# Optimization experiments

Hardware: AMD Instinct MI355X
Metric: run time of the kernel (lower is better)

Reference implementation:

```python
import jax, jax.numpy as jnp
import numpy as np

MAX_POS = 1024  # max_pos_embed_distance
H = 12          # num_heads
D = 768         # input_dim == hidden_dim
P = D // H      # head_dim


def setup_inputs() -> dict:
    key = jax.random.key(0)
    ks = jax.random.split(key, 8)
    s = 1.0 / np.sqrt(D)
    return {
        "x": jax.random.normal(ks[0], (8, 1024, D), dtype=jnp.float32),
        "wq": jax.random.uniform(ks[1], (D, D), jnp.float32, -s, s),
        "bq": jax.random.uniform(ks[2], (D,), jnp.float32, -s, s),
        "wk": jax.random.uniform(ks[3], (D, D), jnp.float32, -s, s),
        "bk": jax.random.uniform(ks[4], (D,), jnp.float32, -s, s),
        "wv": jax.random.uniform(ks[5], (D, D), jnp.float32, -s, s),
        "bv": jax.random.uniform(ks[6], (D,), jnp.float32, -s, s),
        "dist_emb": jax.random.normal(ks[7], (2 * MAX_POS - 1, P), dtype=jnp.float32),
    }


def reference(x, wq, bq, wk, bk, wv, bv, dist_emb):
    b, n, _ = x.shape
    factor = 1.0 / np.sqrt(P)
    # q,k,v: [b, n, h, p]
    q = (x @ wq.T + bq).reshape(b, n, H, P)
    k = (x @ wk.T + bk).reshape(b, n, H, P)
    v = (x @ wv.T + bv).reshape(b, n, H, P)
    raw = jnp.einsum('bihd,bjhd->bhij', q, k)
    # relative-key bias: pos_emb[i, r] = dist_emb[i - r + MAX_POS - 1]
    dist = jnp.arange(n)[:, None] - jnp.arange(n)[None, :]
    pos_emb = dist_emb[dist + MAX_POS - 1]           # [n, n, p]
    raw = raw + jnp.einsum('bihd,ird->bhir', q, pos_emb)
    # NOTE: original scales AFTER adding relative scores
    attn = jax.nn.softmax(raw * factor, axis=-1)
    out = jnp.einsum('bhij,bjhp->bihp', attn, v)
    return out.reshape(b, n, -1)
```

## Files before the change

### kernel.cpp

```cpp
#include <hip/hip_runtime.h>
#include <hip/hip_bf16.h>

#define NH 12
#define HD 64
#define DM 768
#define SEQ 1024
#define BATCH 8

typedef __attribute__((ext_vector_type(8))) short bf16x8;
typedef __attribute__((ext_vector_type(4))) short s16x4;
typedef __attribute__((ext_vector_type(4))) float f32x4;

__device__ __forceinline__ short f2b(float x) {
    unsigned u = __float_as_uint(x);
    u += 0x7fffu + ((u >> 16) & 1u);
    return (short)(u >> 16);
}

#define MFMA(A, B, C) __builtin_amdgcn_mfma_f32_16x16x32_bf16(A, B, C, 0, 0, 0)

__global__ __launch_bounds__(256) void cvt_f32_bf16(
    const float* __restrict__ in, short* __restrict__ out, int n4)
{
    int i = blockIdx.x * 256 + threadIdx.x;
    if (i < n4) {
        f32x4 v = *(const f32x4*)(in + 4 * (size_t)i);
        s16x4 r;
        r[0] = f2b(v[0]); r[1] = f2b(v[1]); r[2] = f2b(v[2]); r[3] = f2b(v[3]);
        *(s16x4*)(out + 4 * (size_t)i) = r;
    }
}

__global__ __launch_bounds__(256, 4) void qkv_mfma(
    const short* __restrict__ xb,
    const short* __restrict__ wqb, const float* __restrict__ bq,
    const short* __restrict__ wkb, const float* __restrict__ bk,
    const short* __restrict__ wvb, const float* __restrict__ bv,
    short* __restrict__ qb, short* __restrict__ kb, short* __restrict__ vt)
{
    __shared__ short Xl[64][72];
    __shared__ short Wl[64][72];

    const int orig = blockIdx.x;
    const int sw   = (orig & 7) * 576 + (orig >> 3);
    const int t    = sw % 36;
    const int by   = t % 12;
    const int z    = t / 12;
    const int bx   = sw / 36;

    const short* wmat = (z == 0) ? wqb : (z == 1) ? wkb : wvb;
    const float* bias = (z == 0) ? bq : (z == 1) ? bk : bv;

    const int i0   = bx * 64;
    const int col0 = by * 64;
    const int tid  = threadIdx.x;
    const int lane = tid & 63;
    const int w    = tid >> 6;
    const int lg   = lane >> 4;
    const int lc   = lane & 15;

    f32x4 acc[4] = {};
    for (int k0 = 0; k0 < DM; k0 += 64) {
        __syncthreads();
        #pragma unroll
        for (int e = tid; e < 512; e += 256) {
            const int r = e >> 3, c8 = e & 7;
            *(bf16x8*)&Xl[r][c8 * 8] =
                *(const bf16x8*)&xb[(size_t)(i0 + r) * DM + k0 + c8 * 8];
            *(bf16x8*)&Wl[r][c8 * 8] =
                *(const bf16x8*)&wmat[(size_t)(col0 + r) * DM + k0 + c8 * 8];
        }
        __syncthreads();
        #pragma unroll
        for (int kh = 0; kh < 2; ++kh) {
            const bf16x8 a = *(const bf16x8*)&Xl[w * 16 + lc][kh * 32 + lg * 8];
            #pragma unroll
            for (int n = 0; n < 4; ++n) {
                const bf16x8 bfr = *(const bf16x8*)&Wl[n * 16 + lc][kh * 32 + lg * 8];
                acc[n] = MFMA(a, bfr, acc[n]);
            }
        }
    }

    if (z < 2) {
        short* outp = (z == 0) ? qb : kb;
        #pragma unroll
        for (int n = 0; n < 4; ++n) {
            const int c = col0 + n * 16 + lc;
            const float bi = bias[c];
            #pragma unroll
            for (int rr = 0; rr < 4; ++rr) {
                const int r = i0 + w * 16 + lg * 4 + rr;
                outp[(size_t)r * DM + c] = f2b(acc[n][rr] + bi);
            }
        }
    } else {
        #pragma unroll
        for (int n = 0; n < 4; ++n) {
            const int c = col0 + n * 16 + lc;
            const int h = c >> 6, d = c & 63;
            const float bi = bias[c];
            #pragma unroll
            for (int rr = 0; rr < 4; ++rr) {
                const int r  = i0 + w * 16 + lg * 4 + rr;
                const int bb = r >> 10, j = r & 1023;
                vt[(((size_t)bb * NH + h) * HD + d) * SEQ + j] = f2b(acc[n][rr] + bi);
            }
        }
    }
}

__global__ __launch_bounds__(512, 4) void attn_flash(
    const short* __restrict__ qb, const short* __restrict__ kb,
    const short* __restrict__ vt, const short* __restrict__ deb,
    float* __restrict__ out)
{
    const int orig = blockIdx.x;
    const int sw   = (orig & 7) * 384 + (orig >> 3);
    const int bx   = sw & 31;
    const int h    = (sw >> 5) % NH;
    const int b    = sw / (32 * NH);

    const int i0   = bx * 32;
    const int tid  = threadIdx.x;
    const int lane = tid & 63;
    const int w    = tid >> 6;
    const int rt   = w >> 2;
    const int js   = w & 3;
    const int lg   = lane >> 4;
    const int lc   = lane & 15;

    __shared__ short Kl[128][72];
    __shared__ short Dl[160][72];
    __shared__ float Tl[32][168];
    __shared__ short Pl[32][136];
    __shared__ float maxp[4][32];
    __shared__ float sump[4][32];

    const short* qrow = qb + ((size_t)(b * SEQ + i0 + rt * 16 + lc)) * DM + h * HD;
    const bf16x8 A0 = *(const bf16x8*)(qrow + lg * 8);
    const bf16x8 A1 = *(const bf16x8*)(qrow + 32 + lg * 8);

    const short* kbase = kb + ((size_t)(b * SEQ)) * DM + h * HD;
    const short* vbase = vt + ((size_t)(b * NH + h) * HD + js * 16 + lc) * SEQ;

    auto stage = [&](int jc) {
        for (int e = tid; e < 128 * 8; e += 512) {
            const int r = e >> 3, c8 = e & 7;
            *(bf16x8*)&Kl[r][c8 * 8] =
                *(const bf16x8*)&kbase[(size_t)(jc + r) * DM + c8 * 8];
        }
        const int wb = i0 - jc + 896;
        for (int e = tid; e < 159 * 8; e += 512) {
            const int r = e >> 3, c8 = e & 7;
            *(bf16x8*)&Dl[r][c8 * 8] =
                *(const bf16x8*)&deb[(size_t)(wb + r) * HD + c8 * 8];
        }
    };

    float m[4], l[4];
    f32x4 O = {0.f, 0.f, 0.f, 0.f};
    #pragma unroll
    for (int rr = 0; rr < 4; ++rr) { m[rr] = -1e30f; l[rr] = 0.f; }

    stage(0);
    __syncthreads();

    for (int c = 0; c < 8; ++c) {
        const int jc = c * 128;

        #pragma unroll
        for (int tt = 0; tt < 3; ++tt) {
            const int ct2 = js + tt * 4;
            if (ct2 < 10) {
                f32x4 a = {0.f, 0.f, 0.f, 0.f};
                a = MFMA(A0, *(const bf16x8*)&Dl[ct2 * 16 + lc][lg * 8], a);
                a = MFMA(A1, *(const bf16x8*)&Dl[ct2 * 16 + lc][32 + lg * 8], a);
                #pragma unroll
                for (int rr = 0; rr < 4; ++rr)
                    Tl[rt * 16 + lg * 4 + rr][ct2 * 16 + lc] = a[rr];
            }
        }
        f32x4 s0 = {0.f, 0.f, 0.f, 0.f}, s1 = {0.f, 0.f, 0.f, 0.f};
        {
            const int j0 = js * 32;
            s0 = MFMA(A0, *(const bf16x8*)&Kl[j0 + lc][lg * 8], s0);
            s0 = MFMA(A1, *(const bf16x8*)&Kl[j0 + lc][32 + lg * 8], s0);
            s1 = MFMA(A0, *(const bf16x8*)&Kl[j0 + 16 + lc][lg * 8], s1);
            s1 = MFMA(A1, *(const bf16x8*)&Kl[j0 + 16 + lc][32 + lg * 8], s1);
        }
        __syncthreads();

        float sv[2][4];
        #pragma unroll
        for (int jt = 0; jt < 2; ++jt)
            #pragma unroll
            for (int rr = 0; rr < 4; ++rr) {
                const int row = rt * 16 + lg * 4 + rr;
                const int jl  = js * 32 + jt * 16 + lc;
                sv[jt][rr] = (jt ? s1[rr] : s0[rr]) + Tl[row][row - jl + 127];
            }
        #pragma unroll
        for (int rr = 0; rr < 4; ++rr) {
            float mw = fmaxf(sv[0][rr], sv[1][rr]);
            mw = fmaxf(mw, __shfl_xor(mw, 1, 64));
            mw = fmaxf(mw, __shfl_xor(mw, 2, 64));
            mw = fmaxf(mw, __shfl_xor(mw, 4, 64));
            mw = fmaxf(mw, __shfl_xor(mw, 8, 64));
            if (lc == 0) maxp[js][rt * 16 + lg * 4 + rr] = mw;
        }
        __syncthreads();

        float scale[4];
        #pragma unroll
        for (int rr = 0; rr < 4; ++rr) {
            const int row = rt * 16 + lg * 4 + rr;
            float mn = m[rr];
            mn = fmaxf(mn, maxp[0][row]);
            mn = fmaxf(mn, maxp[1][row]);
            mn = fmaxf(mn, maxp[2][row]);
            mn = fmaxf(mn, maxp[3][row]);
            scale[rr] = __expf((m[rr] - mn) * 0.125f);
            m[rr] = mn;
            float ps = 0.f;
            #pragma unroll
            for (int jt = 0; jt < 2; ++jt) {
                const float p = __expf((sv[jt][rr] - mn) * 0.125f);
                Pl[row][js * 32 + jt * 16 + lc] = f2b(p);
                ps += p;
            }
            ps += __shfl_xor(ps, 1, 64);
            ps += __shfl_xor(ps, 2, 64);
            ps += __shfl_xor(ps, 4, 64);
            ps += __shfl_xor(ps, 8, 64);
            if (lc == 0) sump[js][row] = ps;
        }
        if (c < 7) stage(jc + 128);
        __syncthreads();

        #pragma unroll
        for (int rr = 0; rr < 4; ++rr) {
            const int row = rt * 16 + lg * 4 + rr;
            l[rr] = l[rr] * scale[rr]
                  + sump[0][row] + sump[1][row] + sump[2][row] + sump[3][row];
            O[rr] *= scale[rr];
        }
        #pragma unroll
        for (int ks = 0; ks < 4; ++ks) {
            const bf16x8 Af = *(const bf16x8*)&Pl[rt * 16 + lc][ks * 32 + lg * 8];
            const bf16x8 Bf = *(const bf16x8*)&vbase[jc + ks * 32 + lg * 8];
            O = MFMA(Af, Bf, O);
        }
    }

    #pragma unroll
    for (int rr = 0; rr < 4; ++rr) {
        const int row = i0 + rt * 16 + lg * 4 + rr;
        out[((size_t)(b * SEQ + row)) * DM + h * HD + js * 16 + lc] = O[rr] / l[rr];
    }
}

extern "C" void kernel_launch(void* const* d_in, const int* in_sizes, int n_in,
                              void* d_out, int out_size, void* d_ws, size_t ws_size,
                              hipStream_t stream) {
    const float* x  = (const float*)d_in[0];
    const float* wq = (const float*)d_in[1];
    const float* bq = (const float*)d_in[2];
    const float* wk = (const float*)d_in[3];
    const float* bk = (const float*)d_in[4];
    const float* wv = (const float*)d_in[5];
    const float* bv = (const float*)d_in[6];
    const float* de = (const float*)d_in[7];
    float* out = (float*)d_out;

    const size_t NX = (size_t)BATCH * SEQ * DM;
    const size_t NW = (size_t)DM * DM;
    const size_t ND = 2047 * HD;
    short* xb  = (short*)d_ws;
    short* wqb = xb  + NX;
    short* wkb = wqb + NW;
    short* wvb = wkb + NW;
    short* deb = wvb + NW;
    short* qbw = deb + ND;
    short* kbw = qbw + NX;
    short* vtw = kbw + NX;

    cvt_f32_bf16<<<(int)((NX / 4 + 255) / 256), 256, 0, stream>>>(x,  xb,  (int)(NX / 4));
    cvt_f32_bf16<<<(int)((NW / 4 + 255) / 256), 256, 0, stream>>>(wq, wqb, (int)(NW / 4));
    cvt_f32_bf16<<<(int)((NW / 4 + 255) / 256), 256, 0, stream>>>(wk, wkb, (int)(NW / 4));
    cvt_f32_bf16<<<(int)((NW / 4 + 255) / 256), 256, 0, stream>>>(wv, wvb, (int)(NW / 4));
    cvt_f32_bf16<<<(int)((ND / 4 + 255) / 256), 256, 0, stream>>>(de, deb, (int)(ND / 4));

    qkv_mfma<<<4608, 256, 0, stream>>>(xb, wqb, bq, wkb, bk, wvb, bv,
                                       qbw, kbw, vtw);
    attn_flash<<<3072, 512, 0, stream>>>(qbw, kbw, vtw, deb, out);
}
```

Measured before the change: 373.2 us.

## Restructure attention to per-wave row ownership with register-shuffled relative bias

The attention kernel now has each block handle 128 query rows, with each of its 8 waves owning 16 rows across all columns. This removes the cross-wave max/sum reductions through shared memory and one barrier per iteration. The relative-position bias tile is kept in registers and redistributed with lane shuffles instead of a float LDS scratch tile. K and distance-embedding staging is software-pipelined through registers into 64-key chunks. The QKV GEMM block is doubled to 128 rows with 512 threads, so each weight tile is reused across more rows. In exchange the attention grid shrinks to 768 blocks and register pressure rises from the four output accumulators.

```diff
diff --git a/kernel.cpp b/kernel.cpp
--- a/kernel.cpp
+++ b/kernel.cpp
@@ -31,18 +31,18 @@
     }
 }
 
-__global__ __launch_bounds__(256, 4) void qkv_mfma(
+__global__ __launch_bounds__(512, 4) void qkv_mfma(
     const short* __restrict__ xb,
     const short* __restrict__ wqb, const float* __restrict__ bq,
     const short* __restrict__ wkb, const float* __restrict__ bk,
     const short* __restrict__ wvb, const float* __restrict__ bv,
     short* __restrict__ qb, short* __restrict__ kb, short* __restrict__ vt)
 {
-    __shared__ short Xl[64][72];
+    __shared__ short Xl[128][72];
     __shared__ short Wl[64][72];
 
     const int orig = blockIdx.x;
-    const int sw   = (orig & 7) * 576 + (orig >> 3);
+    const int sw   = (orig & 7) * 288 + (orig >> 3);
     const int t    = sw % 36;
     const int by   = t % 12;
     const int z    = t / 12;
@@ -51,7 +51,7 @@
     const short* wmat = (z == 0) ? wqb : (z == 1) ? wkb : wvb;
     const float* bias = (z == 0) ? bq : (z == 1) ? bk : bv;
 
-    const int i0   = bx * 64;
+    const int i0   = bx * 128;
     const int col0 = by * 64;
     const int tid  = threadIdx.x;
     const int lane = tid & 63;
@@ -59,17 +59,17 @@
     const int lg   = lane >> 4;
     const int lc   = lane & 15;
 
+    const int sr = tid >> 3, scx = (tid & 7) * 8;
+
     f32x4 acc[4] = {};
     for (int k0 = 0; k0 < DM; k0 += 64) {
         __syncthreads();
-        #pragma unroll
-        for (int e = tid; e < 512; e += 256) {
-            const int r = e >> 3, c8 = e & 7;
-            *(bf16x8*)&Xl[r][c8 * 8] =
-                *(const bf16x8*)&xb[(size_t)(i0 + r) * DM + k0 + c8 * 8];
-            *(bf16x8*)&Wl[r][c8 * 8] =
-                *(const bf16x8*)&wmat[(size_t)(col0 + r) * DM + k0 + c8 * 8];
-        }
+        *(bf16x8*)&Xl[sr][scx] =
+            *(const bf16x8*)&xb[(size_t)(i0 + sr) * DM + k0 + scx];
+        *(bf16x8*)&Xl[sr + 64][scx] =
+            *(const bf16x8*)&xb[(size_t)(i0 + 64 + sr) * DM + k0 + scx];
+        *(bf16x8*)&Wl[sr][scx] =
+            *(const bf16x8*)&wmat[(size_t)(col0 + sr) * DM + k0 + scx];
         __syncthreads();
         #pragma unroll
         for (int kh = 0; kh < 2; ++kh) {
@@ -116,147 +116,164 @@
     float* __restrict__ out)
 {
     const int orig = blockIdx.x;
-    const int sw   = (orig & 7) * 384 + (orig >> 3);
-    const int bx   = sw & 31;
-    const int h    = (sw >> 5) % NH;
-    const int b    = sw / (32 * NH);
-
-    const int i0   = bx * 32;
+    const int sw   = (orig & 7) * 96 + (orig >> 3);
+    const int bx   = sw & 7;
+    const int rest = sw >> 3;
+    const int h    = rest % NH;
+    const int b    = rest / NH;
+
+    const int i0   = bx * 128;
     const int tid  = threadIdx.x;
     const int lane = tid & 63;
     const int w    = tid >> 6;
-    const int rt   = w >> 2;
-    const int js   = w & 3;
+    const int wR   = w * 16;
     const int lg   = lane >> 4;
     const int lc   = lane & 15;
 
-    __shared__ short Kl[128][72];
-    __shared__ short Dl[160][72];
-    __shared__ float Tl[32][168];
-    __shared__ short Pl[32][136];
-    __shared__ float maxp[4][32];
-    __shared__ float sump[4][32];
-
-    const short* qrow = qb + ((size_t)(b * SEQ + i0 + rt * 16 + lc)) * DM + h * HD;
+    __shared__ short Kl[64][72];
+    __shared__ short Dl[192][72];
+    __shared__ short Pl[8][16][136];
+
+    const short* qrow = qb + ((size_t)(b * SEQ + i0 + wR + lc)) * DM + h * HD;
     const bf16x8 A0 = *(const bf16x8*)(qrow + lg * 8);
     const bf16x8 A1 = *(const bf16x8*)(qrow + 32 + lg * 8);
 
-    const short* kbase = kb + ((size_t)(b * SEQ)) * DM + h * HD;
-    const short* vbase = vt + ((size_t)(b * NH + h) * HD + js * 16 + lc) * SEQ;
-
-    auto stage = [&](int jc) {
-        for (int e = tid; e < 128 * 8; e += 512) {
-            const int r = e >> 3, c8 = e & 7;
-            *(bf16x8*)&Kl[r][c8 * 8] =
-                *(const bf16x8*)&kbase[(size_t)(jc + r) * DM + c8 * 8];
-        }
-        const int wb = i0 - jc + 896;
-        for (int e = tid; e < 159 * 8; e += 512) {
-            const int r = e >> 3, c8 = e & 7;
-            *(bf16x8*)&Dl[r][c8 * 8] =
-                *(const bf16x8*)&deb[(size_t)(wb + r) * HD + c8 * 8];
-        }
+    const short* kbase = kb + (size_t)(b * SEQ) * DM + h * HD;
+    const short* vbase = vt + ((size_t)(b * NH + h) * HD) * SEQ;
+
+    const int sr = tid >> 3, scx = (tid & 7) * 8;
+    bf16x8 kreg, dreg0, dreg1, dreg2;
+
+    auto stage_load = [&](int jc) {
+        kreg = *(const bf16x8*)&kbase[(size_t)(jc + sr) * DM + scx];
+        const int wb = i0 - jc + 960;
+        const int r2 = min(wb + sr + 128, 2046);
+        dreg0 = *(const bf16x8*)&deb[(size_t)(wb + sr) * HD + scx];
+        dreg1 = *(const bf16x8*)&deb[(size_t)(wb + sr + 64) * HD + scx];
+        dreg2 = *(const bf16x8*)&deb[(size_t)r2 * HD + scx];
     };
+    auto stage_store = [&]() {
+        *(bf16x8*)&Kl[sr][scx]       = kreg;
+        *(bf16x8*)&Dl[sr][scx]       = dreg0;
+        *(bf16x8*)&Dl[sr + 64][scx]  = dreg1;
+        *(bf16x8*)&Dl[sr + 128][scx] = dreg2;
+    };
 
     float m[4], l[4];
-    f32x4 O = {0.f, 0.f, 0.f, 0.f};
+    f32x4 O0 = {0.f,0.f,0.f,0.f}, O1 = {0.f,0.f,0.f,0.f};
+    f32x4 O2 = {0.f,0.f,0.f,0.f}, O3 = {0.f,0.f,0.f,0.f};
     #pragma unroll
     for (int rr = 0; rr < 4; ++rr) { m[rr] = -1e30f; l[rr] = 0.f; }
 
-    stage(0);
+    stage_load(0);
+    stage_store();
     __syncthreads();
 
-    for (int c = 0; c < 8; ++c) {
-        const int jc = c * 128;
-
-        #pragma unroll
-        for (int tt = 0; tt < 3; ++tt) {
-            const int ct2 = js + tt * 4;
-            if (ct2 < 10) {
-                f32x4 a = {0.f, 0.f, 0.f, 0.f};
-                a = MFMA(A0, *(const bf16x8*)&Dl[ct2 * 16 + lc][lg * 8], a);
-                a = MFMA(A1, *(const bf16x8*)&Dl[ct2 * 16 + lc][32 + lg * 8], a);
-                #pragma unroll
-                for (int rr = 0; rr < 4; ++rr)
-                    Tl[rt * 16 + lg * 4 + rr][ct2 * 16 + lc] = a[rr];
-            }
-        }
-        f32x4 s0 = {0.f, 0.f, 0.f, 0.f}, s1 = {0.f, 0.f, 0.f, 0.f};
+    for (int c = 0; c < 16; ++c) {
+        const int jc = c * 64;
+        if (c < 15) stage_load(jc + 64);
+
+        f32x4 T0, T1, T2, T3, T4;
         {
-            const int j0 = js * 32;
-            s0 = MFMA(A0, *(const bf16x8*)&Kl[j0 + lc][lg * 8], s0);
-            s0 = MFMA(A1, *(const bf16x8*)&Kl[j0 + lc][32 + lg * 8], s0);
-            s1 = MFMA(A0, *(const bf16x8*)&Kl[j0 + 16 + lc][lg * 8], s1);
-            s1 = MFMA(A1, *(const bf16x8*)&Kl[j0 + 16 + lc][32 + lg * 8], s1);
+            f32x4 a;
+            a = f32x4{0.f,0.f,0.f,0.f};
+            a = MFMA(A0, *(const bf16x8*)&Dl[wR + 0*16 + lc][lg*8], a);
+            T0 = MFMA(A1, *(const bf16x8*)&Dl[wR + 0*16 + lc][32 + lg*8], a);
+            a = f32x4{0.f,0.f,0.f,0.f};
+            a = MFMA(A0, *(const bf16x8*)&Dl[wR + 1*16 + lc][lg*8], a);
+            T1 = MFMA(A1, *(const bf16x8*)&Dl[wR + 1*16 + lc][32 + lg*8], a);
+            a = f32x4{0.f,0.f,0.f,0.f};
+            a = MFMA(A0, *(const bf16x8*)&Dl[wR + 2*16 + lc][lg*8], a);
+            T2 = MFMA(A1, *(const bf16x8*)&Dl[wR + 2*16 + lc][32 + lg*8], a);
+            a = f32x4{0.f,0.f,0.f,0.f};
+            a = MFMA(A0, *(const bf16x8*)&Dl[wR + 3*16 + lc][lg*8], a);
+            T3 = MFMA(A1, *(const bf16x8*)&Dl[wR + 3*16 + lc][32 + lg*8], a);
+            a = f32x4{0.f,0.f,0.f,0.f};
+            a = MFMA(A0, *(const bf16x8*)&Dl[wR + 4*16 + lc][lg*8], a);
+            T4 = MFMA(A1, *(const bf16x8*)&Dl[wR + 4*16 + lc][32 + lg*8], a);
+        }
+
+        f32x4 sv[4];
+        #pragma unroll
+        for (int jt = 0; jt < 4; ++jt) {
+            f32x4 s = {0.f,0.f,0.f,0.f};
+            s = MFMA(A0, *(const bf16x8*)&Kl[jt*16 + lc][lg*8], s);
+            s = MFMA(A1, *(const bf16x8*)&Kl[jt*16 + lc][32 + lg*8], s);
+            sv[jt] = s;
         }
         __syncthreads();
 
-        float sv[2][4];
-        #pragma unroll
-        for (int jt = 0; jt < 2; ++jt)
+        float mw[4] = {-1e30f, -1e30f, -1e30f, -1e30f};
+        #pragma unroll
+        for (int jt = 0; jt < 4; ++jt) {
             #pragma unroll
             for (int rr = 0; rr < 4; ++rr) {
-                const int row = rt * 16 + lg * 4 + rr;
-                const int jl  = js * 32 + jt * 16 + lc;
-                sv[jt][rr] = (jt ? s1[rr] : s0[rr]) + Tl[row][row - jl + 127];
-            }
+                const int loff = 63 + lg * 4 + rr - jt * 16 - lc;
+                const int src  = (lane & 48) | (loff & 15);
+                float c0, c1;
+                if (jt == 0)      { c0 = __shfl(T3[rr], src, 64); c1 = __shfl(T4[rr], src, 64); }
+                else if (jt == 1) { c0 = __shfl(T2[rr], src, 64); c1 = __shfl(T3[rr], src, 64); }
+                else if (jt == 2) { c0 = __shfl(T1[rr], src, 64); c1 = __shfl(T2[rr], src, 64); }
+                else              { c0 = __shfl(T0[rr], src, 64); c1 = __shfl(T1[rr], src, 64); }
+                const int tlo = 3 - jt;
+                float bias = ((loff >> 4) == tlo) ? c0 : c1;
+                sv[jt][rr] += bias;
+                mw[rr] = fmaxf(mw[rr], sv[jt][rr]);
+            }
+        }
+
+        float scale[4];
         #pragma unroll
         for (int rr = 0; rr < 4; ++rr) {
-            float mw = fmaxf(sv[0][rr], sv[1][rr]);
-            mw = fmaxf(mw, __shfl_xor(mw, 1, 64));
-            mw = fmaxf(mw, __shfl_xor(mw, 2, 64));
-            mw = fmaxf(mw, __shfl_xor(mw, 4, 64));
-            mw = fmaxf(mw, __shfl_xor(mw, 8, 64));
-            if (lc == 0) maxp[js][rt * 16 + lg * 4 + rr] = mw;
-        }
-        __syncthreads();
-
-        float scale[4];
-        #pragma unroll
-        for (int rr = 0; rr < 4; ++rr) {
-            const int row = rt * 16 + lg * 4 + rr;
-            float mn = m[rr];
-            mn = fmaxf(mn, maxp[0][row]);
-            mn = fmaxf(mn, maxp[1][row]);
-            mn = fmaxf(mn, maxp[2][row]);
-            mn = fmaxf(mn, maxp[3][row]);
+            float v = mw[rr];
+            v = fmaxf(v, __shfl_xor(v, 1, 64));
+            v = fmaxf(v, __shfl_xor(v, 2, 64));
+            v = fmaxf(v, __shfl_xor(v, 4, 64));
+            v = fmaxf(v, __shfl_xor(v, 8, 64));
+            const float mn = fmaxf(m[rr], v);
             scale[rr] = __expf((m[rr] - mn) * 0.125f);
             m[rr] = mn;
-            float ps = 0.f;
-            #pragma unroll
-            for (int jt = 0; jt < 2; ++jt) {
+            float s = 0.f;
+            #pragma unroll
+            for (int jt = 0; jt < 4; ++jt) {
                 const float p = __expf((sv[jt][rr] - mn) * 0.125f);
-                Pl[row][js * 32 + jt * 16 + lc] = f2b(p);
-                ps += p;
-            }
-            ps += __shfl_xor(ps, 1, 64);
-            ps += __shfl_xor(ps, 2, 64);
-            ps += __shfl_xor(ps, 4, 64);
-            ps += __shfl_xor(ps, 8, 64);
-            if (lc == 0) sump[js][row] = ps;
-        }
-        if (c < 7) stage(jc + 128);
+                Pl[w][lg * 4 + rr][jt * 16 + lc] = f2b(p);
+                s += p;
+            }
+            s += __shfl_xor(s, 1, 64);
+            s += __shfl_xor(s, 2, 64);
+            s += __shfl_xor(s, 4, 64);
+            s += __shfl_xor(s, 8, 64);
+            l[rr] = l[rr] * scale[rr] + s;
+        }
+
+        if (c < 15) stage_store();
+
+        #pragma unroll
+        for (int rr = 0; rr < 4; ++rr) {
+            O0[rr] *= scale[rr]; O1[rr] *= scale[rr];
+            O2[rr] *= scale[rr]; O3[rr] *= scale[rr];
+        }
+        #pragma unroll
+        for (int ks = 0; ks < 2; ++ks) {
+            const bf16x8 Af = *(const bf16x8*)&Pl[w][lc][ks * 32 + lg * 8];
+            const size_t vo = jc + ks * 32 + lg * 8;
+            O0 = MFMA(Af, *(const bf16x8*)&vbase[(size_t)( 0 + lc) * SEQ + vo], O0);
+            O1 = MFMA(Af, *(const bf16x8*)&vbase[(size_t)(16 + lc) * SEQ + vo], O1);
+            O2 = MFMA(Af, *(const bf16x8*)&vbase[(size_t)(32 + lc) * SEQ + vo], O2);
+            O3 = MFMA(Af, *(const bf16x8*)&vbase[(size_t)(48 + lc) * SEQ + vo], O3);
+        }
         __syncthreads();
-
-        #pragma unroll
-        for (int rr = 0; rr < 4; ++rr) {
-            const int row = rt * 16 + lg * 4 + rr;
-            l[rr] = l[rr] * scale[rr]
-                  + sump[0][row] + sump[1][row] + sump[2][row] + sump[3][row];
-            O[rr] *= scale[rr];
-        }
-        #pragma unroll
-        for (int ks = 0; ks < 4; ++ks) {
-            const bf16x8 Af = *(const bf16x8*)&Pl[rt * 16 + lc][ks * 32 + lg * 8];
-            const bf16x8 Bf = *(const bf16x8*)&vbase[jc + ks * 32 + lg * 8];
-            O = MFMA(Af, Bf, O);
-        }
     }
 
     #pragma unroll
     for (int rr = 0; rr < 4; ++rr) {
-        const int row = i0 + rt * 16 + lg * 4 + rr;
-        out[((size_t)(b * SEQ + row)) * DM + h * HD + js * 16 + lc] = O[rr] / l[rr];
+        const size_t rowoff = ((size_t)(b * SEQ + i0 + wR + lg * 4 + rr)) * DM + h * HD;
+        const float inv = 1.0f / l[rr];
+        out[rowoff +  0 + lc] = O0[rr] * inv;
+        out[rowoff + 16 + lc] = O1[rr] * inv;
+        out[rowoff + 32 + lc] = O2[rr] * inv;
+        out[rowoff + 48 + lc] = O3[rr] * inv;
     }
 }
 
@@ -291,7 +308,7 @@
     cvt_f32_bf16<<<(int)((NW / 4 + 255) / 256), 256, 0, stream>>>(wv, wvb, (int)(NW / 4));
     cvt_f32_bf16<<<(int)((ND / 4 + 255) / 256), 256, 0, stream>>>(de, deb, (int)(ND / 4));
 
-    qkv_mfma<<<4608, 256, 0, stream>>>(xb, wqb, bq, wkb, bk, wvb, bv,
+    qkv_mfma<<<2304, 512, 0, stream>>>(xb, wqb, bq, wkb, bk, wvb, bv,
                                        qbw, kbw, vtw);
-    attn_flash<<<3072, 512, 0, stream>>>(qbw, kbw, vtw, deb, out);
-}
+    attn_flash<<<768, 512, 0, stream>>>(qbw, kbw, vtw, deb, out);
+}
```

After: 383.4 us. 2.7% more time.
